# Kernel optimization log

Measured on AMD Instinct MI355X. Metric: run time of the kernel, lower is better.

## Reference

```python
import jax, jax.numpy as jnp
import numpy as np
import math

INPUT_DIM = 1024
HIDDEN = 1024
BATCH = 64
SEQ = 512


def setup_inputs() -> dict:
    key = jax.random.key(0)
    ks = jax.random.split(key, 6)
    stdv = 1.0 / math.sqrt(HIDDEN)
    u = lambda k, shape: jax.random.uniform(k, shape, jnp.float32, -stdv, stdv)
    return {
        "inputs": jax.random.normal(ks[0], (BATCH, SEQ, INPUT_DIM), jnp.float32),
        "h0": jax.random.normal(ks[1], (1, BATCH, HIDDEN), jnp.float32),
        "weight_ih": u(ks[2], (3 * HIDDEN, INPUT_DIM)),
        "weight_hh": u(ks[3], (3 * HIDDEN, HIDDEN)),
        "bias_ih": u(ks[4], (3 * HIDDEN,)),
        "bias_hh": u(ks[5], (3 * HIDDEN,)),
    }


def reference(inputs, h0, weight_ih, weight_hh, bias_ih, bias_hh):
    # inputs: [b, s, I]; h0: [1, b, H]; weight_ih: [3H, I]; weight_hh: [3H, H]
    H = h0.shape[-1]
    # Precompute input projections for all timesteps in one big GEMM: [b, s, 3H]
    x_proj = jnp.einsum("bsi,gi->bsg", inputs, weight_ih) + bias_ih
    # Split hidden weights/biases into r, z, n gate blocks (rows 0:H, H:2H, 2H:3H)
    whr, whz, whn = weight_hh[:H], weight_hh[H:2 * H], weight_hh[2 * H:]
    bhr, bhz, bhn = bias_hh[:H], bias_hh[H:2 * H], bias_hh[2 * H:]

    def step(h, xg):
        # h: [b, H]; xg: [b, 3H] (precomputed x@W_ih.T + b_ih for this timestep)
        xr, xz, xn = xg[:, :H], xg[:, H:2 * H], xg[:, 2 * H:]
        r = jax.nn.sigmoid(xr + h @ whr.T + bhr)
        z = jax.nn.sigmoid(xz + h @ whz.T + bhz)
        n = jnp.tanh(xn + r * (h @ whn.T + bhn))
        h_new = (1.0 - z) * n + z * h
        return h_new, h_new

    hn, outs = jax.lax.scan(step, h0[0], jnp.swapaxes(x_proj, 0, 1))  # scan over seq
    outputs = jnp.swapaxes(outs, 0, 1)  # [b, s, H]
    return outputs, hn[None]  # hn: [1, b, H]
```

## Files before the change

kernel.cpp:

```cpp
#include <hip/hip_runtime.h>

#define BB 64
#define HH 1024
#define SS 512

typedef __attribute__((ext_vector_type(8))) short short8;
typedef __attribute__((ext_vector_type(4))) float f32x4;
typedef __attribute__((ext_vector_type(4))) unsigned u32x4;
typedef unsigned long long u64;

__device__ __forceinline__ unsigned short f2bf(float f) {
  union { float f; unsigned u; } v; v.f = f;
  unsigned r = v.u + 0x7fffu + ((v.u >> 16) & 1u);
  return (unsigned short)(r >> 16);
}

__global__ void gru_prep(const float* __restrict__ wih, const float* __restrict__ whh,
                         const float* __restrict__ h0, const float* __restrict__ x,
                         unsigned short* __restrict__ wih_bf,
                         unsigned short* __restrict__ whh_bf,
                         unsigned* __restrict__ htag,
                         unsigned short* __restrict__ xbf, int do_x) {
  const int NT = gridDim.x * blockDim.x;
  const int tid = blockIdx.x * blockDim.x + threadIdx.x;
  for (int i = tid; i < 3 * HH * HH; i += NT) {
    wih_bf[i] = f2bf(wih[i]);
    whh_bf[i] = f2bf(whh[i]);
  }
  for (int i = tid; i < BB * HH; i += NT) {
    htag[i]           = (unsigned)f2bf(h0[i]);
    htag[BB * HH + i] = 0xFFFF0000u;
  }
  if (do_x)
    for (int i = tid; i < BB * SS * HH; i += NT) xbf[i] = f2bf(x[i]);
}

__global__ __launch_bounds__(256, 1) void gru_main(
    const float* __restrict__ x, const unsigned short* __restrict__ xbf, const int use_xbf,
    const float* __restrict__ h0,
    const float* __restrict__ bih, const float* __restrict__ bhh,
    const unsigned short* __restrict__ wih_bf, const unsigned short* __restrict__ whh_bf,
    unsigned* __restrict__ htag, float* __restrict__ out) {
  __shared__ f32x4 ldsv[2 * 4 * 4 * 64];

  const int wg   = blockIdx.x;
  const int idx  = (wg >> 3) + (wg & 7) * 32;
  const int c0   = (idx >> 2) * 16;
  const int m0   = (idx & 3) * 16;
  const int wv   = threadIdx.x >> 6;
  const int ln   = threadIdx.x & 63;
  const int l15  = ln & 15;
  const int quad = ln >> 4;
  const int kb   = wv * 256 + quad * 8;

  const unsigned short* wib = wih_bf + (size_t)(c0 + l15) * HH + kb;
  const unsigned short* whb = whh_bf + (size_t)(c0 + l15) * HH + kb;
  short8 Wi[3][8], Wh[3][8];
#pragma unroll
  for (int g = 0; g < 3; ++g)
#pragma unroll
    for (int kk = 0; kk < 8; ++kk) {
      Wi[g][kk] = *(const short8*)(wib + (size_t)g * HH * HH + kk * 32);
      Wh[g][kk] = *(const short8*)(whb + (size_t)g * HH * HH + kk * 32);
    }

  const int j = c0 + l15;
  const float br   = bih[j] + bhh[j];
  const float bz   = bih[HH + j] + bhh[HH + j];
  const float bi_n = bih[2 * HH + j];
  const float bh_n = bhh[2 * HH + j];

  const int brow = m0 + wv * 4 + quad;
  float hreg = h0[brow * HH + j];

  const float*          xfp = x   + (size_t)(m0 + l15) * (SS * HH) + kb;
  const unsigned short* xbp = xbf + (size_t)(m0 + l15) * (SS * HH) + kb;
  const int hw_off = (m0 + l15) * HH + kb;

#define LOAD_AX(tt)                                                          \
  if (use_xbf) {                                                             \
    const unsigned short* xp = xbp + (size_t)(tt) * HH;                      \
    _Pragma("unroll")                                                        \
    for (int kk = 0; kk < 8; ++kk) ax[kk] = *(const short8*)(xp + kk * 32);  \
  } else {                                                                   \
    const float* xp = xfp + (size_t)(tt) * HH;                               \
    _Pragma("unroll")                                                        \
    for (int kk = 0; kk < 8; ++kk) {                                         \
      float4 xa = *(const float4*)(xp + kk * 32);                            \
      float4 xb = *(const float4*)(xp + kk * 32 + 4);                        \
      short8 v;                                                              \
      v[0] = (short)f2bf(xa.x); v[1] = (short)f2bf(xa.y);                    \
      v[2] = (short)f2bf(xa.z); v[3] = (short)f2bf(xa.w);                    \
      v[4] = (short)f2bf(xb.x); v[5] = (short)f2bf(xb.y);                    \
      v[6] = (short)f2bf(xb.z); v[7] = (short)f2bf(xb.w);                    \
      ax[kk] = v;                                                            \
    }                                                                        \
  }

#define HLOAD(i, off)                                                        \
  asm volatile("global_load_dwordx4 %0, %1, off offset:" #off " sc0 sc1"     \
               : "=v"(hr[i]) : "v"(hb))
#define ISSUE_H()                                                            \
  do {                                                                       \
    HLOAD(0, 0);    HLOAD(1, 16);   HLOAD(2, 128);  HLOAD(3, 144);           \
    HLOAD(4, 256);  HLOAD(5, 272);  HLOAD(6, 384);  HLOAD(7, 400);           \
    HLOAD(8, 512);  HLOAD(9, 528);  HLOAD(10, 640); HLOAD(11, 656);          \
    HLOAD(12, 768); HLOAD(13, 784); HLOAD(14, 896); HLOAD(15, 912);          \
  } while (0)

  short8 ax[8];
  LOAD_AX(0);

#pragma unroll 1
  for (int t = 0; t < SS; ++t) {
    const int buf = (t & 1) * (4 * 4 * 64);
    const unsigned tagv = (unsigned)t << 16;
    const unsigned* hb = htag + (t & 1) * (BB * HH) + hw_off;

    u32x4 hr[16];
    ISSUE_H();

    f32x4 a0 = {0.f, 0.f, 0.f, 0.f}, a1 = a0, a2 = a0;
#pragma unroll
    for (int kk = 0; kk < 8; ++kk) {
      a0 = __builtin_amdgcn_mfma_f32_16x16x32_bf16(ax[kk], Wi[0][kk], a0, 0, 0, 0);
      a1 = __builtin_amdgcn_mfma_f32_16x16x32_bf16(ax[kk], Wi[1][kk], a1, 0, 0, 0);
      a2 = __builtin_amdgcn_mfma_f32_16x16x32_bf16(ax[kk], Wi[2][kk], a2, 0, 0, 0);
    }

#pragma unroll 1
    for (int round = 0;; ++round) {
      asm volatile("s_waitcnt vmcnt(0)" ::: "memory");
      __builtin_amdgcn_sched_barrier(0);
      unsigned bad = 0;
#pragma unroll
      for (int i = 0; i < 16; ++i)
        bad |= (hr[i][0] ^ tagv) | (hr[i][1] ^ tagv) |
               (hr[i][2] ^ tagv) | (hr[i][3] ^ tagv);
      const int ok = ((bad & 0xFFFF0000u) == 0);
      if (__all(ok) || round >= 2048) break;
      ISSUE_H();
    }

    if (t + 1 < SS) { LOAD_AX(t + 1); }

    f32x4 a3 = {0.f, 0.f, 0.f, 0.f}, a4 = a3, a5 = a3;
#pragma unroll
    for (int kk = 0; kk < 8; ++kk) {
      unsigned p0 = __builtin_amdgcn_perm(hr[2 * kk][1],     hr[2 * kk][0],     0x05040100u);
      unsigned p1 = __builtin_amdgcn_perm(hr[2 * kk][3],     hr[2 * kk][2],     0x05040100u);
      unsigned p2 = __builtin_amdgcn_perm(hr[2 * kk + 1][1], hr[2 * kk + 1][0], 0x05040100u);
      unsigned p3 = __builtin_amdgcn_perm(hr[2 * kk + 1][3], hr[2 * kk + 1][2], 0x05040100u);
      union { unsigned u[4]; short8 s; } uu = {{p0, p1, p2, p3}};
      a3 = __builtin_amdgcn_mfma_f32_16x16x32_bf16(uu.s, Wh[0][kk], a3, 0, 0, 0);
      a4 = __builtin_amdgcn_mfma_f32_16x16x32_bf16(uu.s, Wh[1][kk], a4, 0, 0, 0);
      a5 = __builtin_amdgcn_mfma_f32_16x16x32_bf16(uu.s, Wh[2][kk], a5, 0, 0, 0);
    }
    a0 += a3;
    a1 += a4;

    ldsv[buf + (wv * 4 + 0) * 64 + ln] = a0;
    ldsv[buf + (wv * 4 + 1) * 64 + ln] = a1;
    ldsv[buf + (wv * 4 + 2) * 64 + ln] = a2;
    ldsv[buf + (wv * 4 + 3) * 64 + ln] = a5;
    __syncthreads();

    {
      const float* lf = (const float*)(ldsv + buf);
      float s0 = 0.f, s1 = 0.f, s2 = 0.f, s3 = 0.f;
#pragma unroll
      for (int sw = 0; sw < 4; ++sw) {
        const int base = (sw * 4 * 64 + wv * 16 + l15) * 4 + quad;
        s0 += lf[base];       s1 += lf[base + 256];
        s2 += lf[base + 512]; s3 += lf[base + 768];
      }
      float r = 1.f / (1.f + __expf(-(s0 + br)));
      float z = 1.f / (1.f + __expf(-(s1 + bz)));
      float pre = s2 + bi_n + r * (s3 + bh_n);
      float e2 = __expf(2.f * pre);
      float n = 1.f - 2.f / (e2 + 1.f);
      float hnew = (1.f - z) * n + z * hreg;
      hreg = hnew;
      if (t + 1 < SS) {
        unsigned pk = (unsigned)f2bf(hnew) | ((unsigned)(t + 1) << 16);
        __hip_atomic_store(htag + ((t + 1) & 1) * (BB * HH) + brow * HH + j, pk,
                           __ATOMIC_RELAXED, __HIP_MEMORY_SCOPE_AGENT);
      }
      __builtin_nontemporal_store(hnew,
          &out[(size_t)brow * (SS * HH) + (size_t)t * HH + j]);
      if (t == SS - 1)
        __builtin_nontemporal_store(hnew, &out[(size_t)BB * SS * HH + brow * HH + j]);
    }
  }
#undef LOAD_AX
#undef HLOAD
#undef ISSUE_H
}

extern "C" void kernel_launch(void* const* d_in, const int* in_sizes, int n_in,
                              void* d_out, int out_size, void* d_ws, size_t ws_size,
                              hipStream_t stream) {
  const float* x   = (const float*)d_in[0];
  const float* h0  = (const float*)d_in[1];
  const float* wih = (const float*)d_in[2];
  const float* whh = (const float*)d_in[3];
  const float* bih = (const float*)d_in[4];
  const float* bhh = (const float*)d_in[5];
  float* out = (float*)d_out;

  char* ws = (char*)d_ws;
  const size_t off_whh = 6291456;
  const size_t off_h   = 12582912;
  const size_t off_x   = 13107200;
  const size_t need_x  = off_x + (size_t)BB * SS * HH * 2;

  unsigned short* wih_bf = (unsigned short*)ws;
  unsigned short* whh_bf = (unsigned short*)(ws + off_whh);
  unsigned*       htag   = (unsigned*)(ws + off_h);
  unsigned short* xbf    = (unsigned short*)(ws + off_x);
  const int use_xbf = (ws_size >= need_x) ? 1 : 0;

  hipLaunchKernelGGL(gru_prep, dim3(2048), dim3(256), 0, stream,
                     wih, whh, h0, x, wih_bf, whh_bf, htag, xbf, use_xbf);
  hipLaunchKernelGGL(gru_main, dim3(256), dim3(256), 0, stream,
                     x, xbf, use_xbf, h0, bih, bhh, wih_bf, whh_bf, htag, out);
}
```

Measured before the change: 3.081 ms.

## Prefetch next-step hidden state right after publishing and restructure LDS reduction

Issues the hidden-state polling loads for step t+1 right after the thread publishes its own h, so the first probe overlaps the output store and the next input-projection MFMAs. Readiness is now checked with a min-reduction against a monotonically increasing tag, and later polling rounds back off with s_sleep. Input loads become asm loads so the vmcnt accounting works, and the LDS layout is transposed so each thread reads its four gate partials as float4 vectors. The cost is fragile manual vmcnt counting, including a dummy load added to keep the count right, and the chance that early probes return stale data and need re-polling.

```diff
diff --git a/kernel.cpp b/kernel.cpp
--- a/kernel.cpp
+++ b/kernel.cpp
@@ -29,7 +29,7 @@
   }
   for (int i = tid; i < BB * HH; i += NT) {
     htag[i]           = (unsigned)f2bf(h0[i]);
-    htag[BB * HH + i] = 0xFFFF0000u;
+    htag[BB * HH + i] = 0u;
   }
   if (do_x)
     for (int i = tid; i < BB * SS * HH; i += NT) xbf[i] = f2bf(x[i]);
@@ -41,7 +41,7 @@
     const float* __restrict__ bih, const float* __restrict__ bhh,
     const unsigned short* __restrict__ wih_bf, const unsigned short* __restrict__ whh_bf,
     unsigned* __restrict__ htag, float* __restrict__ out) {
-  __shared__ f32x4 ldsv[2 * 4 * 4 * 64];
+  __shared__ f32x4 ldsv[2 * 4 * 256];
 
   const int wg   = blockIdx.x;
   const int idx  = (wg >> 3) + (wg & 7) * 32;
@@ -52,6 +52,7 @@
   const int l15  = ln & 15;
   const int quad = ln >> 4;
   const int kb   = wv * 256 + quad * 8;
+  const int tid  = threadIdx.x;
 
   const unsigned short* wib = wih_bf + (size_t)(c0 + l15) * HH + kb;
   const unsigned short* whb = whh_bf + (size_t)(c0 + l15) * HH + kb;
@@ -77,11 +78,14 @@
   const unsigned short* xbp = xbf + (size_t)(m0 + l15) * (SS * HH) + kb;
   const int hw_off = (m0 + l15) * HH + kb;
 
-#define LOAD_AX(tt)                                                          \
+#define XL(i, off)                                                           \
+  asm volatile("global_load_dwordx4 %0, %1, off offset:" #off " sc0"         \
+               : "=v"(ax[i]) : "v"(xp))
+#define ISSUE_AX(tt)                                                         \
   if (use_xbf) {                                                             \
     const unsigned short* xp = xbp + (size_t)(tt) * HH;                      \
-    _Pragma("unroll")                                                        \
-    for (int kk = 0; kk < 8; ++kk) ax[kk] = *(const short8*)(xp + kk * 32);  \
+    XL(0, 0);   XL(1, 64);  XL(2, 128); XL(3, 192);                          \
+    XL(4, 256); XL(5, 320); XL(6, 384); XL(7, 448);                          \
   } else {                                                                   \
     const float* xp = xfp + (size_t)(tt) * HH;                               \
     _Pragma("unroll")                                                        \
@@ -97,29 +101,63 @@
     }                                                                        \
   }
 
-#define HLOAD(i, off)                                                        \
+#define HL(i, off)                                                           \
   asm volatile("global_load_dwordx4 %0, %1, off offset:" #off " sc0 sc1"     \
                : "=v"(hr[i]) : "v"(hb))
-#define ISSUE_H()                                                            \
+#define ISSUE_H(hb)                                                          \
   do {                                                                       \
-    HLOAD(0, 0);    HLOAD(1, 16);   HLOAD(2, 128);  HLOAD(3, 144);           \
-    HLOAD(4, 256);  HLOAD(5, 272);  HLOAD(6, 384);  HLOAD(7, 400);           \
-    HLOAD(8, 512);  HLOAD(9, 528);  HLOAD(10, 640); HLOAD(11, 656);          \
-    HLOAD(12, 768); HLOAD(13, 784); HLOAD(14, 896); HLOAD(15, 912);          \
+    HL(0, 0);    HL(1, 16);   HL(2, 128);  HL(3, 144);                       \
+    HL(4, 256);  HL(5, 272);  HL(6, 384);  HL(7, 400);                       \
+    HL(8, 512);  HL(9, 528);  HL(10, 640); HL(11, 656);                      \
+    HL(12, 768); HL(13, 784); HL(14, 896); HL(15, 912);                      \
   } while (0)
 
+#define HCHECK(okv)                                                          \
+  {                                                                          \
+    unsigned q_[16];                                                         \
+    _Pragma("unroll")                                                        \
+    for (int i_ = 0; i_ < 16; ++i_) {                                        \
+      unsigned a_ = hr[i_][0] < hr[i_][1] ? hr[i_][0] : hr[i_][1];           \
+      unsigned b_ = hr[i_][2] < hr[i_][3] ? hr[i_][2] : hr[i_][3];           \
+      q_[i_] = a_ < b_ ? a_ : b_;                                            \
+    }                                                                        \
+    _Pragma("unroll")                                                        \
+    for (int s_ = 8; s_ > 0; s_ >>= 1)                                       \
+      for (int i_ = 0; i_ < s_; ++i_)                                        \
+        q_[i_] = q_[i_] < q_[i_ + s_] ? q_[i_] : q_[i_ + s_];                \
+    okv = (q_[0] >= tagv);                                                   \
+  }
+
+#define HMFMA()                                                              \
+  _Pragma("unroll")                                                          \
+  for (int kk = 0; kk < 8; ++kk) {                                           \
+    unsigned p0 = __builtin_amdgcn_perm(hr[2*kk][1],   hr[2*kk][0],   0x05040100u); \
+    unsigned p1 = __builtin_amdgcn_perm(hr[2*kk][3],   hr[2*kk][2],   0x05040100u); \
+    unsigned p2 = __builtin_amdgcn_perm(hr[2*kk+1][1], hr[2*kk+1][0], 0x05040100u); \
+    unsigned p3 = __builtin_amdgcn_perm(hr[2*kk+1][3], hr[2*kk+1][2], 0x05040100u); \
+    union { unsigned u[4]; short8 s; } uu = {{p0, p1, p2, p3}};              \
+    a3 = __builtin_amdgcn_mfma_f32_16x16x32_bf16(uu.s, Wh[0][kk], a3, 0, 0, 0); \
+    a4 = __builtin_amdgcn_mfma_f32_16x16x32_bf16(uu.s, Wh[1][kk], a4, 0, 0, 0); \
+    a5 = __builtin_amdgcn_mfma_f32_16x16x32_bf16(uu.s, Wh[2][kk], a5, 0, 0, 0); \
+  }
+
   short8 ax[8];
-  LOAD_AX(0);
+  u32x4 hr[16];
+
+  ISSUE_AX(0);
+  {
+    const unsigned* hb = htag + hw_off;
+    ISSUE_H(hb);
+    u32x4 dj;
+    asm volatile("global_load_dwordx4 %0, %1, off sc0 sc1" : "=v"(dj) : "v"(hb));
+  }
 
 #pragma unroll 1
   for (int t = 0; t < SS; ++t) {
-    const int buf = (t & 1) * (4 * 4 * 64);
     const unsigned tagv = (unsigned)t << 16;
-    const unsigned* hb = htag + (t & 1) * (BB * HH) + hw_off;
-
-    u32x4 hr[16];
-    ISSUE_H();
-
+
+    asm volatile("s_waitcnt vmcnt(17)" ::: "memory");
+    __builtin_amdgcn_sched_barrier(0);
     f32x4 a0 = {0.f, 0.f, 0.f, 0.f}, a1 = a0, a2 = a0;
 #pragma unroll
     for (int kk = 0; kk < 8; ++kk) {
@@ -128,73 +166,73 @@
       a2 = __builtin_amdgcn_mfma_f32_16x16x32_bf16(ax[kk], Wi[2][kk], a2, 0, 0, 0);
     }
 
+    {
+      int ok;
+      asm volatile("s_waitcnt vmcnt(1)" ::: "memory");
+      __builtin_amdgcn_sched_barrier(0);
+      HCHECK(ok);
+      if (!__all(ok)) {
+        const unsigned* hb = htag + (t & 1) * (BB * HH) + hw_off;
 #pragma unroll 1
-    for (int round = 0;; ++round) {
-      asm volatile("s_waitcnt vmcnt(0)" ::: "memory");
-      __builtin_amdgcn_sched_barrier(0);
-      unsigned bad = 0;
-#pragma unroll
-      for (int i = 0; i < 16; ++i)
-        bad |= (hr[i][0] ^ tagv) | (hr[i][1] ^ tagv) |
-               (hr[i][2] ^ tagv) | (hr[i][3] ^ tagv);
-      const int ok = ((bad & 0xFFFF0000u) == 0);
-      if (__all(ok) || round >= 2048) break;
-      ISSUE_H();
-    }
-
-    if (t + 1 < SS) { LOAD_AX(t + 1); }
+        for (int round = 0; round < 4096; ++round) {
+          ISSUE_H(hb);
+          asm volatile("s_waitcnt vmcnt(0)" ::: "memory");
+          __builtin_amdgcn_sched_barrier(0);
+          HCHECK(ok);
+          if (__all(ok)) break;
+          if (round > 7) __builtin_amdgcn_s_sleep(1);
+        }
+      }
+    }
+
+    if (t + 1 < SS) { ISSUE_AX(t + 1); }
 
     f32x4 a3 = {0.f, 0.f, 0.f, 0.f}, a4 = a3, a5 = a3;
-#pragma unroll
-    for (int kk = 0; kk < 8; ++kk) {
-      unsigned p0 = __builtin_amdgcn_perm(hr[2 * kk][1],     hr[2 * kk][0],     0x05040100u);
-      unsigned p1 = __builtin_amdgcn_perm(hr[2 * kk][3],     hr[2 * kk][2],     0x05040100u);
-      unsigned p2 = __builtin_amdgcn_perm(hr[2 * kk + 1][1], hr[2 * kk + 1][0], 0x05040100u);
-      unsigned p3 = __builtin_amdgcn_perm(hr[2 * kk + 1][3], hr[2 * kk + 1][2], 0x05040100u);
-      union { unsigned u[4]; short8 s; } uu = {{p0, p1, p2, p3}};
-      a3 = __builtin_amdgcn_mfma_f32_16x16x32_bf16(uu.s, Wh[0][kk], a3, 0, 0, 0);
-      a4 = __builtin_amdgcn_mfma_f32_16x16x32_bf16(uu.s, Wh[1][kk], a4, 0, 0, 0);
-      a5 = __builtin_amdgcn_mfma_f32_16x16x32_bf16(uu.s, Wh[2][kk], a5, 0, 0, 0);
-    }
+    HMFMA();
     a0 += a3;
     a1 += a4;
 
-    ldsv[buf + (wv * 4 + 0) * 64 + ln] = a0;
-    ldsv[buf + (wv * 4 + 1) * 64 + ln] = a1;
-    ldsv[buf + (wv * 4 + 2) * 64 + ln] = a2;
-    ldsv[buf + (wv * 4 + 3) * 64 + ln] = a5;
+    {
+      f32x4* P = ldsv + (t & 1) * 1024 + wv * 256;
+#pragma unroll
+      for (int i = 0; i < 4; ++i) {
+        f32x4 v = {a0[i], a1[i], a2[i], a5[i]};
+        P[quad * 64 + i * 16 + l15] = v;
+      }
+    }
     __syncthreads();
 
     {
-      const float* lf = (const float*)(ldsv + buf);
-      float s0 = 0.f, s1 = 0.f, s2 = 0.f, s3 = 0.f;
-#pragma unroll
-      for (int sw = 0; sw < 4; ++sw) {
-        const int base = (sw * 4 * 64 + wv * 16 + l15) * 4 + quad;
-        s0 += lf[base];       s1 += lf[base + 256];
-        s2 += lf[base + 512]; s3 += lf[base + 768];
-      }
-      float r = 1.f / (1.f + __expf(-(s0 + br)));
-      float z = 1.f / (1.f + __expf(-(s1 + bz)));
-      float pre = s2 + bi_n + r * (s3 + bh_n);
+      const f32x4* P = ldsv + (t & 1) * 1024;
+      f32x4 sv = P[tid] + P[256 + tid] + P[512 + tid] + P[768 + tid];
+      float r = 1.f / (1.f + __expf(-(sv[0] + br)));
+      float z = 1.f / (1.f + __expf(-(sv[1] + bz)));
+      float pre = sv[2] + bi_n + r * (sv[3] + bh_n);
       float e2 = __expf(2.f * pre);
       float n = 1.f - 2.f / (e2 + 1.f);
       float hnew = (1.f - z) * n + z * hreg;
       hreg = hnew;
+
       if (t + 1 < SS) {
         unsigned pk = (unsigned)f2bf(hnew) | ((unsigned)(t + 1) << 16);
         __hip_atomic_store(htag + ((t + 1) & 1) * (BB * HH) + brow * HH + j, pk,
                            __ATOMIC_RELAXED, __HIP_MEMORY_SCOPE_AGENT);
+        const unsigned* hb = htag + ((t + 1) & 1) * (BB * HH) + hw_off;
+        ISSUE_H(hb);
       }
+      asm volatile("" ::: "memory");
       __builtin_nontemporal_store(hnew,
           &out[(size_t)brow * (SS * HH) + (size_t)t * HH + j]);
       if (t == SS - 1)
         __builtin_nontemporal_store(hnew, &out[(size_t)BB * SS * HH + brow * HH + j]);
     }
   }
-#undef LOAD_AX
-#undef HLOAD
+#undef XL
+#undef ISSUE_AX
+#undef HL
 #undef ISSUE_H
+#undef HCHECK
+#undef HMFMA
 }
 
 extern "C" void kernel_launch(void* const* d_in, const int* in_sizes, int n_in,
```

Result: slower. 4.080 ms (+32.4%).
